# Kernel optimization log

Hardware: AMD Instinct MI355X
Metric: run time of the kernel (lower is better)

## Reference

```python
import jax, jax.numpy as jnp
import numpy as np
from jax import lax

B, D, H, W = 8, 256, 56, 56
DH = 32            # d_head
HEADS = D // DH    # 8
WIN = 7            # window size
TOPK = 8           # top-k windows
DM = 4 * D         # mlp hidden = 1024
EPS = 1e-5


def bn(x, g, b, m, v):
    # inference-mode BatchNorm2d over channel dim of NCHW
    return g[:, None, None] * (x - m[:, None, None]) * lax.rsqrt(v[:, None, None] + EPS) + b[:, None, None]


def conv1x1(x, w):
    return jnp.einsum('bchw,oc->bohw', x, w)


def setup_inputs() -> dict:
    key = jax.random.key(0)
    ks = jax.random.split(key, 24)
    s = 0.05
    return {
        'x': jax.random.normal(ks[0], (B, D, H, W), jnp.float32),
        'g1': jax.random.uniform(ks[1], (D,)) + 0.5,
        'b1': jax.random.normal(ks[2], (D,)) * s,
        'm1': jax.random.normal(ks[3], (D,)) * s,
        'v1': jax.random.uniform(ks[4], (D,)) + 0.5,
        'W_qkv': jax.random.normal(ks[5], (3 * D, D)) * s,
        'W_merge': jax.random.normal(ks[6], (D, D)) * s,
        'b_merge': jax.random.normal(ks[7], (D,)) * s,
        'W1': jax.random.normal(ks[8], (DM, D)) * s,
        'g2': jax.random.uniform(ks[9], (DM,)) + 0.5,
        'b2': jax.random.normal(ks[10], (DM,)) * s,
        'm2': jax.random.normal(ks[11], (DM,)) * s,
        'v2': jax.random.uniform(ks[12], (DM,)) + 0.5,
        'Wdw': jax.random.normal(ks[13], (DM, 1, 3, 3)) * s,
        'g3': jax.random.uniform(ks[14], (DM,)) + 0.5,
        'b3': jax.random.normal(ks[15], (DM,)) * s,
        'm3': jax.random.normal(ks[16], (DM,)) * s,
        'v3': jax.random.uniform(ks[17], (DM,)) + 0.5,
        'W2': jax.random.normal(ks[18], (D, DM)) * s,
        'g4': jax.random.uniform(ks[19], (D,)) + 0.5,
        'b4': jax.random.normal(ks[20], (D,)) * s,
        'm4': jax.random.normal(ks[21], (D,)) * s,
        'v4': jax.random.uniform(ks[22], (D,)) + 0.5,
    }


def _forward(x, g1, b1, m1, v1, W_qkv, W_merge, b_merge,
             W1, g2, b2, m2, v2, Wdw, g3, b3, m3, v3, W2, g4, b4, m4, v4):
    b_, d, Hh, Ww = x.shape
    nh, nw = Hh // WIN, Ww // WIN
    nWnd, ww = nh * nw, WIN * WIN

    # qkv projection: BN -> GELU -> 1x1 conv
    h = jax.nn.gelu(bn(x, g1, b1, m1, v1), approximate=False)
    qkv = conv1x1(h, W_qkv)
    q, k, v = jnp.split(qkv, 3, axis=1)  # each [b, d, H, W]

    def part(t):  # -> [b, heads, nWnd, ww, dh]
        t = t.reshape(b_, HEADS, DH, nh, WIN, nw, WIN)
        return jnp.transpose(t, (0, 1, 3, 5, 4, 6, 2)).reshape(b_, HEADS, nWnd, ww, DH)

    qw, kw, vw = part(q), part(k), part(v)

    # window-level routing: mean-pooled q/k per window, top-k window selection
    def pool(t):  # [b, d, H, W] -> [b, nWnd, d]
        t = t.reshape(b_, d, nh, WIN, nw, WIN).mean(axis=(3, 5))
        return t.reshape(b_, d, nWnd).transpose(0, 2, 1)

    qr, kr = pool(q), pool(k)
    aff = jnp.einsum('bnd,bmd->bnm', qr, kr)        # [b, nWnd, nWnd]
    idx = lax.top_k(aff, TOPK)[1]                    # [b, nWnd, TOPK]

    def gath(t, i):  # t [heads, nWnd, ww, dh], i [nWnd, TOPK]
        return t[:, i]  # [heads, nWnd, TOPK, ww, dh]

    kg = jax.vmap(gath)(kw, idx).reshape(b_, HEADS, nWnd, TOPK * ww, DH)
    vg = jax.vmap(gath)(vw, idx).reshape(b_, HEADS, nWnd, TOPK * ww, DH)

    scores = jnp.einsum('bhnqd,bhnkd->bhnqk', qw, kg) / jnp.sqrt(jnp.float32(DH))
    attn = jax.nn.softmax(scores, axis=-1)
    out = jnp.einsum('bhnqk,bhnkd->bhnqd', attn, vg)  # [b, heads, nWnd, ww, dh]

    # un-partition back to [b, d, H, W]
    out = out.reshape(b_, HEADS, nh, nw, WIN, WIN, DH)
    msg = jnp.transpose(out, (0, 1, 6, 2, 4, 3, 5)).reshape(b_, d, Hh, Ww)

    # merge (1x1 conv with bias) + residual
    x = x + conv1x1(msg, W_merge) + b_merge[None, :, None, None]

    # MB mlp block: 1x1 -> BN -> GELU -> dw3x3 -> BN -> GELU -> 1x1 -> BN
    h2 = conv1x1(x, W1)
    h2 = jax.nn.gelu(bn(h2, g2, b2, m2, v2), approximate=False)
    h2 = lax.conv_general_dilated(h2, Wdw, (1, 1), 'SAME',
                                  feature_group_count=DM,
                                  dimension_numbers=('NCHW', 'OIHW', 'NCHW'))
    h2 = jax.nn.gelu(bn(h2, g3, b3, m3, v3), approximate=False)
    h2 = conv1x1(h2, W2)
    h2 = bn(h2, g4, b4, m4, v4)
    return x + h2


def reference(x, g1, b1, m1, v1, W_qkv, W_merge, b_merge,
              W1, g2, b2, m2, v2, Wdw, g3, b3, m3, v3, W2, g4, b4, m4, v4):
    return _forward(x, g1, b1, m1, v1, W_qkv, W_merge, b_merge,
                    W1, g2, b2, m2, v2, Wdw, g3, b3, m3, v3, W2, g4, b4, m4, v4)
```

## Files before the change

kernel.cpp:

```cpp
#include <hip/hip_runtime.h>
#include <hip/hip_bf16.h>
#include <cstdint>
#include <cstddef>

#define BB 8
#define PP 3136
#define EPSV 1e-5f
#define SCQK 0.17677669529663687f

using bf16x8 = __attribute__((ext_vector_type(8))) short;
using f32x4  = __attribute__((ext_vector_type(4))) float;

__device__ __forceinline__ float bf2f(unsigned short u) {
    union { float f; unsigned int i; } c; c.i = ((unsigned int)u) << 16; return c.f;
}
__device__ __forceinline__ unsigned short f2bf(float f) {
    __hip_bfloat16 h = __float2bfloat16(f);
    union { __hip_bfloat16 h; unsigned short u; } c; c.h = h; return c.u;
}
__device__ __forceinline__ float gelu_f(float t) {
    return 0.5f * t * (1.0f + erff(t * 0.70710678118654752440f));
}
__device__ __forceinline__ float gelu_fast(float x) {
    float z = 1.5957691216057308f * (x + 0.044715f * x * x * x);
    return x / (1.0f + __expf(-z));
}
__device__ __forceinline__ void async16(const void* g, void* s) {
    __builtin_amdgcn_global_load_lds(
        (const __attribute__((address_space(1))) unsigned int*)g,
        (__attribute__((address_space(3))) unsigned int*)s, 16, 0, 0);
}
__device__ __forceinline__ uint4 pack8(const float* v) {
    uint4 o;
    o.x = (unsigned)f2bf(v[0]) | ((unsigned)f2bf(v[1]) << 16);
    o.y = (unsigned)f2bf(v[2]) | ((unsigned)f2bf(v[3]) << 16);
    o.z = (unsigned)f2bf(v[4]) | ((unsigned)f2bf(v[5]) << 16);
    o.w = (unsigned)f2bf(v[6]) | ((unsigned)f2bf(v[7]) << 16);
    return o;
}

__global__ __launch_bounds__(256) void cvt_all_k(
    const float* __restrict__ Wq, const float* __restrict__ Wm,
    const float* __restrict__ W1, const float* __restrict__ W2,
    unsigned short* __restrict__ dq, unsigned short* __restrict__ dm,
    unsigned short* __restrict__ d1, unsigned short* __restrict__ d2)
{
    int i = blockIdx.x * 256 + threadIdx.x;
    if (i < 196608) dq[i] = f2bf(Wq[i]);
    else if (i < 262144) dm[i - 196608] = f2bf(Wm[i - 196608]);
    else if (i < 524288) d1[i - 262144] = f2bf(W1[i - 262144]);
    else d2[i - 524288] = f2bf(W2[i - 524288]);
}

__global__ __launch_bounds__(256) void transin_k(const float* __restrict__ x,
    const float* __restrict__ g1, const float* __restrict__ b1,
    const float* __restrict__ m1, const float* __restrict__ v1,
    float* __restrict__ x_pm, unsigned short* __restrict__ h_bf)
{
    __shared__ float tile[64][65];
    __shared__ float gam[64], bet[64], mu[64], rst[64];
    const int p0 = blockIdx.x * 64, c0 = blockIdx.y * 64, b = blockIdx.z;
    const int t = threadIdx.x;
    if (t < 64) { int c = c0 + t; gam[t] = g1[c]; bet[t] = b1[c]; mu[t] = m1[c]; rst[t] = rsqrtf(v1[c] + EPSV); }
    {
        int cl = t >> 2, px = (t & 3) * 16;
        const float* src = x + ((size_t)(b * 256 + c0 + cl)) * PP + p0 + px;
        #pragma unroll
        for (int i4 = 0; i4 < 4; i4++) {
            float4 r0 = *(const float4*)(src + i4 * 4);
            tile[cl][px + i4*4 + 0] = r0.x; tile[cl][px + i4*4 + 1] = r0.y;
            tile[cl][px + i4*4 + 2] = r0.z; tile[cl][px + i4*4 + 3] = r0.w;
        }
    }
    __syncthreads();
    {
        int pl = t >> 2, cb = (t & 3) * 16;
        float raw[16], hg[16];
        #pragma unroll
        for (int i = 0; i < 16; i++) {
            float vv = tile[cb + i][pl];
            raw[i] = vv;
            hg[i] = gelu_fast(gam[cb + i] * (vv - mu[cb + i]) * rst[cb + i] + bet[cb + i]);
        }
        size_t off = ((size_t)b * PP + p0 + pl) * 256 + c0 + cb;
        float* xd = x_pm + off;
        #pragma unroll
        for (int i4 = 0; i4 < 4; i4++) {
            float4 o; o.x = raw[i4*4]; o.y = raw[i4*4+1]; o.z = raw[i4*4+2]; o.w = raw[i4*4+3];
            *(float4*)(xd + i4 * 4) = o;
        }
        uint4* hd = (uint4*)(h_bf + off);
        hd[0] = pack8(&hg[0]);
        hd[1] = pack8(&hg[8]);
    }
}

template<int EPI>
__global__ __launch_bounds__(256) void gemm_mfma_k(
    const unsigned short* __restrict__ Aact,
    const unsigned short* __restrict__ Wbf,
    const int K, const int Mout,
    void* __restrict__ C1, void* __restrict__ C2,
    const float* __restrict__ e0, const float* __restrict__ e1,
    const float* __restrict__ e2, const float* __restrict__ e3,
    const float* __restrict__ resid)
{
    __shared__ __align__(16) char smem[32768];
    unsigned short* As0 = (unsigned short*)smem;
    unsigned short* Bs0 = (unsigned short*)(smem + 16384);
    float* T = (float*)smem;

    const int tid = threadIdx.x;
    const int w = tid >> 6, lane = tid & 63, g = lane >> 4, l15 = lane & 15;
    const int wm = w >> 1, wn = w & 1;
    const size_t row0 = (size_t)blockIdx.x * 128;
    const int n0 = blockIdx.y * 128;
    const int srow = tid >> 2, scb = tid & 3;

    const f32x4 vzero = {0.f, 0.f, 0.f, 0.f};
    f32x4 acc[4][4];
    #pragma unroll
    for (int mf = 0; mf < 4; mf++)
        #pragma unroll
        for (int nf = 0; nf < 4; nf++) acc[mf][nf] = vzero;

    const int NT = K >> 5;

    auto STAGE = [&](int s) {
        const int k0 = s << 5;
        unsigned short* Ad = As0 + (s & 1) * 4096;
        unsigned short* Bd = Bs0 + (s & 1) * 4096;
        #pragma unroll
        for (int r = 0; r < 2; r++) {
            int row = r * 64 + srow;
            int cbp = scb ^ ((row >> 1) & 3);
            async16(Aact + (row0 + row) * K + k0 + cbp * 8, Ad + r * 2048 + w * 512);
            async16(Wbf + (size_t)(n0 + row) * K + k0 + cbp * 8, Bd + r * 2048 + w * 512);
        }
    };
    auto COMPUTE = [&](int t) {
        const unsigned short* Ab = As0 + (t & 1) * 4096;
        const unsigned short* Bb = Bs0 + (t & 1) * 4096;
        bf16x8 af[4], bfr[4];
        #pragma unroll
        for (int mf = 0; mf < 4; mf++) {
            int row = wm * 64 + mf * 16 + l15;
            int gb = g ^ ((row >> 1) & 3);
            af[mf] = *(const bf16x8*)&Ab[row * 32 + gb * 8];
        }
        #pragma unroll
        for (int nf = 0; nf < 4; nf++) {
            int row = wn * 64 + nf * 16 + l15;
            int gb = g ^ ((row >> 1) & 3);
            bfr[nf] = *(const bf16x8*)&Bb[row * 32 + gb * 8];
        }
        #pragma unroll
        for (int mf = 0; mf < 4; mf++)
            #pragma unroll
            for (int nf = 0; nf < 4; nf++)
                acc[mf][nf] = __builtin_amdgcn_mfma_f32_16x16x32_bf16(af[mf], bfr[nf], acc[mf][nf], 0, 0, 0);
    };

    STAGE(0);
    for (int t = 0; t < NT; ++t) {
        __syncthreads();
        if (t + 1 < NT) STAGE(t + 1);
        COMPUTE(t);
    }

    __syncthreads();
    const int r32 = tid >> 3;
    const int col0 = (tid & 7) * 16;
    #pragma unroll
    for (int p = 0; p < 4; ++p) {
        if (p) __syncthreads();
        if (wm == (p >> 1)) {
            const int mfb = (p & 1) * 2;
            #pragma unroll
            for (int mo = 0; mo < 2; mo++)
                #pragma unroll
                for (int nf = 0; nf < 4; nf++)
                    #pragma unroll
                    for (int r = 0; r < 4; r++)
                        T[(mo * 16 + g * 4 + r) * 132 + wn * 64 + nf * 16 + l15] = acc[mfb + mo][nf][r];
        }
        __syncthreads();
        float vals[16];
        #pragma unroll
        for (int i = 0; i < 4; i++) {
            float4 v = *(const float4*)&T[r32 * 132 + col0 + i * 4];
            vals[i*4+0] = v.x; vals[i*4+1] = v.y; vals[i*4+2] = v.z; vals[i*4+3] = v.w;
        }
        const size_t prow = row0 + p * 32 + r32;
        const int mc0 = n0 + col0;
        const size_t off = prow * Mout + mc0;
        if (EPI == 0) {
            const float s = (mc0 < 256) ? SCQK : 1.0f;
            #pragma unroll
            for (int j = 0; j < 16; j++) vals[j] *= s;
            uint4* dst = (uint4*)((unsigned short*)C1 + off);
            dst[0] = pack8(&vals[0]); dst[1] = pack8(&vals[8]);
        } else if (EPI == 1) {
            #pragma unroll
            for (int i = 0; i < 4; i++) {
                float4 bi = *(const float4*)(e0 + mc0 + i * 4);
                float4 rr = *(const float4*)(resid + off + i * 4);
                vals[i*4+0] += bi.x + rr.x; vals[i*4+1] += bi.y + rr.y;
                vals[i*4+2] += bi.z + rr.z; vals[i*4+3] += bi.w + rr.w;
            }
            float4* d1 = (float4*)((float*)C1 + off);
            #pragma unroll
            for (int i = 0; i < 4; i++) {
                float4 o; o.x = vals[i*4]; o.y = vals[i*4+1]; o.z = vals[i*4+2]; o.w = vals[i*4+3];
                d1[i] = o;
            }
            uint4* d2 = (uint4*)((unsigned short*)C2 + off);
            d2[0] = pack8(&vals[0]); d2[1] = pack8(&vals[8]);
        } else if (EPI == 2) {
            #pragma unroll
            for (int i = 0; i < 4; i++) {
                float4 ga = *(const float4*)(e0 + mc0 + i * 4);
                float4 be = *(const float4*)(e1 + mc0 + i * 4);
                float4 mm = *(const float4*)(e2 + mc0 + i * 4);
                float4 vv = *(const float4*)(e3 + mc0 + i * 4);
                vals[i*4+0] = gelu_fast(ga.x * (vals[i*4+0] - mm.x) * rsqrtf(vv.x + EPSV) + be.x);
                vals[i*4+1] = gelu_fast(ga.y * (vals[i*4+1] - mm.y) * rsqrtf(vv.y + EPSV) + be.y);
                vals[i*4+2] = gelu_fast(ga.z * (vals[i*4+2] - mm.z) * rsqrtf(vv.z + EPSV) + be.z);
                vals[i*4+3] = gelu_fast(ga.w * (vals[i*4+3] - mm.w) * rsqrtf(vv.w + EPSV) + be.w);
            }
            uint4* dst = (uint4*)((unsigned short*)C1 + off);
            dst[0] = pack8(&vals[0]); dst[1] = pack8(&vals[8]);
        } else {
            #pragma unroll
            for (int i = 0; i < 4; i++) {
                float4 ga = *(const float4*)(e0 + mc0 + i * 4);
                float4 be = *(const float4*)(e1 + mc0 + i * 4);
                float4 mm = *(const float4*)(e2 + mc0 + i * 4);
                float4 vv = *(const float4*)(e3 + mc0 + i * 4);
                float4 rr = *(const float4*)(resid + off + i * 4);
                vals[i*4+0] = ga.x * (vals[i*4+0] - mm.x) * rsqrtf(vv.x + EPSV) + be.x + rr.x;
                vals[i*4+1] = ga.y * (vals[i*4+1] - mm.y) * rsqrtf(vv.y + EPSV) + be.y + rr.y;
                vals[i*4+2] = ga.z * (vals[i*4+2] - mm.z) * rsqrtf(vv.z + EPSV) + be.z + rr.z;
                vals[i*4+3] = ga.w * (vals[i*4+3] - mm.w) * rsqrtf(vv.w + EPSV) + be.w + rr.w;
            }
            float4* d1 = (float4*)((float*)C1 + off);
            #pragma unroll
            for (int i = 0; i < 4; i++) {
                float4 o; o.x = vals[i*4]; o.y = vals[i*4+1]; o.z = vals[i*4+2]; o.w = vals[i*4+3];
                d1[i] = o;
            }
        }
    }
}

__global__ __launch_bounds__(256) void poolh_k(const float* __restrict__ x_pm,
    const float* __restrict__ g1, const float* __restrict__ b1,
    const float* __restrict__ m1, const float* __restrict__ v1,
    float* __restrict__ ph)
{
    __shared__ float part[4][256];
    __shared__ float gam[256], bet[256], mu[256], rst[256];
    const int n = blockIdx.x, b = blockIdx.y, t = threadIdx.x;
    gam[t] = g1[t]; bet[t] = b1[t]; mu[t] = m1[t]; rst[t] = rsqrtf(v1[t] + EPSV);
    __syncthreads();
    const int c4 = (t & 63) * 4, pg = t >> 6;
    float s0 = 0.f, s1 = 0.f, s2 = 0.f, s3 = 0.f;
    for (int j = pg; j < 49; j += 4) {
        int p = ((n >> 3) * 7 + j / 7) * 56 + (n & 7) * 7 + j % 7;
        float4 vx = *(const float4*)(x_pm + ((size_t)b * PP + p) * 256 + c4);
        s0 += gelu_f(gam[c4+0] * (vx.x - mu[c4+0]) * rst[c4+0] + bet[c4+0]);
        s1 += gelu_f(gam[c4+1] * (vx.y - mu[c4+1]) * rst[c4+1] + bet[c4+1]);
        s2 += gelu_f(gam[c4+2] * (vx.z - mu[c4+2]) * rst[c4+2] + bet[c4+2]);
        s3 += gelu_f(gam[c4+3] * (vx.w - mu[c4+3]) * rst[c4+3] + bet[c4+3]);
    }
    part[pg][c4 + 0] = s0; part[pg][c4 + 1] = s1; part[pg][c4 + 2] = s2; part[pg][c4 + 3] = s3;
    __syncthreads();
    float tot = part[0][t] + part[1][t] + part[2][t] + part[3][t];
    ph[((size_t)b * 64 + n) * 256 + t] = tot * (1.0f / 49.0f);
}

__global__ __launch_bounds__(256) void qrkr_k(const float* __restrict__ ph,
    const float* __restrict__ Wqkv, float* __restrict__ qr, float* __restrict__ kr)
{
    __shared__ float row[256];
    const int n = blockIdx.x, b = blockIdx.y, t = threadIdx.x;
    row[t] = ph[((size_t)b * 64 + n) * 256 + t];
    __syncthreads();
    const float* wq = Wqkv + (size_t)t * 256;
    const float* wk = Wqkv + (size_t)(256 + t) * 256;
    float aq = 0.f, ak = 0.f;
    #pragma unroll 4
    for (int k = 0; k < 256; k += 4) {
        float4 a4 = *(const float4*)(wq + k);
        float4 b4 = *(const float4*)(wk + k);
        aq += row[k]*a4.x + row[k+1]*a4.y + row[k+2]*a4.z + row[k+3]*a4.w;
        ak += row[k]*b4.x + row[k+1]*b4.y + row[k+2]*b4.z + row[k+3]*b4.w;
    }
    qr[((size_t)b * 64 + n) * 256 + t] = aq;
    kr[((size_t)b * 64 + n) * 256 + t] = ak;
}

__global__ __launch_bounds__(64) void topk_k(const float* __restrict__ qr,
    const float* __restrict__ kr, int* __restrict__ idxb)
{
    const int n = blockIdx.x, b_ = blockIdx.y;
    const int tid = threadIdx.x;
    __shared__ float qrow[256];
    *reinterpret_cast<float4*>(&qrow[tid * 4]) =
        *reinterpret_cast<const float4*>(qr + ((size_t)(b_ * 64) + n) * 256 + tid * 4);
    __syncthreads();
    const float* kp = kr + ((size_t)(b_ * 64) + tid) * 256;
    float av = 0.f;
    #pragma unroll 4
    for (int c = 0; c < 256; c++) av = fmaf(qrow[c], kp[c], av);
    for (int t = 0; t < 8; t++) {
        float v = av; int id = tid;
        #pragma unroll
        for (int off = 32; off; off >>= 1) {
            float v2 = __shfl_xor(v, off);
            int id2 = __shfl_xor(id, off);
            if (v2 > v || (v2 == v && id2 < id)) { v = v2; id = id2; }
        }
        if (tid == 0) idxb[((b_ * 64) + n) * 8 + t] = id;
        if (tid == id) av = -1e30f;
    }
}

__global__ __launch_bounds__(256) void attn_mfma_k(const unsigned short* __restrict__ qkv,
    const int* __restrict__ idxb, unsigned short* __restrict__ msg)
{
    __shared__ __align__(16) unsigned short Vt[32 * 72];
    __shared__ __align__(16) unsigned short Pr[4][16 * 72];
    const int n = blockIdx.x, h = blockIdx.y, b = blockIdx.z;
    const int tid = threadIdx.x;
    const int w = tid >> 6, lane = tid & 63, g = lane >> 4, l15 = lane & 15;

    for (int e = tid; e < 32 * 72; e += 256) Vt[e] = 0;

    const int iq = w * 16 + l15;
    bf16x8 qf = {0, 0, 0, 0, 0, 0, 0, 0};
    if (iq < 49) {
        int p = ((n >> 3) * 7 + iq / 7) * 56 + (n & 7) * 7 + iq % 7;
        qf = *(const bf16x8*)(qkv + ((size_t)b * PP + p) * 768 + h * 32 + g * 8);
    }
    int widx[8];
    {
        const int* ip = idxb + ((b * 64) + n) * 8;
        #pragma unroll
        for (int t = 0; t < 8; t++) widx[t] = ip[t];
    }
    const f32x4 vzero = {0.f, 0.f, 0.f, 0.f};
    f32x4 o0 = vzero, o1 = vzero;
    float mrow = -1e30f, lrow = 0.f;

    const bool act = tid < 196;
    const int jrow = tid >> 2, c8 = (tid & 3) * 8;
    uint4 vv_r = {0,0,0,0};
    auto LOADV = [&](int t) {
        int wsrc = widx[t];
        int p = ((wsrc >> 3) * 7 + jrow / 7) * 56 + (wsrc & 7) * 7 + jrow % 7;
        vv_r = *(const uint4*)(qkv + ((size_t)b * PP + p) * 768 + 512 + h * 32 + c8);
    };
    if (act) LOADV(0);

    for (int t = 0; t < 8; t++) {
        const int wsrc = widx[t];
        const int sy0 = (wsrc >> 3) * 7, sx0 = (wsrc & 7) * 7;
        bf16x8 kf[4];
        #pragma unroll
        for (int nf = 0; nf < 4; nf++) {
            int j = nf * 16 + l15;
            int jc = (j < 49) ? j : 0;
            int p = (sy0 + jc / 7) * 56 + sx0 + jc % 7;
            kf[nf] = *(const bf16x8*)(qkv + ((size_t)b * PP + p) * 768 + 256 + h * 32 + g * 8);
        }
        __syncthreads();
        if (act) {
            const unsigned short* pv = (const unsigned short*)&vv_r;
            #pragma unroll
            for (int jj = 0; jj < 8; jj++) {
                int dh = c8 + jj;
                Vt[dh * 72 + (jrow ^ (((dh >> 3) & 3) << 3))] = pv[jj];
            }
            if (t < 7) LOADV(t + 1);
        }
        __syncthreads();
        f32x4 s[4];
        #pragma unroll
        for (int nf = 0; nf < 4; nf++)
            s[nf] = __builtin_amdgcn_mfma_f32_16x16x32_bf16(kf[nf], qf, vzero, 0, 0, 0);
        float sv[16];
        #pragma unroll
        for (int nf = 0; nf < 4; nf++)
            #pragma unroll
            for (int r = 0; r < 4; r++) {
                int j = nf * 16 + g * 4 + r;
                sv[nf * 4 + r] = (j < 49) ? s[nf][r] : -1e30f;
            }
        float wmx = sv[0];
        #pragma unroll
        for (int e = 1; e < 16; e++) wmx = fmaxf(wmx, sv[e]);
        wmx = fmaxf(wmx, __shfl_xor(wmx, 16));
        wmx = fmaxf(wmx, __shfl_xor(wmx, 32));
        float mn = fmaxf(mrow, wmx);
        float corr = __expf(mrow - mn);
        mrow = mn;
        float rsum = 0.f;
        #pragma unroll
        for (int e = 0; e < 16; e++) { float pe = __expf(sv[e] - mn); sv[e] = pe; rsum += pe; }
        rsum += __shfl_xor(rsum, 16);
        rsum += __shfl_xor(rsum, 32);
        lrow = lrow * corr + rsum;
        #pragma unroll
        for (int r = 0; r < 4; r++) { o0[r] *= corr; o1[r] *= corr; }
        #pragma unroll
        for (int nf = 0; nf < 4; nf++) {
            uint2 pw;
            pw.x = (unsigned)f2bf(sv[nf*4+0]) | ((unsigned)f2bf(sv[nf*4+1]) << 16);
            pw.y = (unsigned)f2bf(sv[nf*4+2]) | ((unsigned)f2bf(sv[nf*4+3]) << 16);
            *(uint2*)&Pr[w][l15 * 72 + nf * 16 + g * 4] = pw;
        }
        asm volatile("s_waitcnt lgkmcnt(0)" ::: "memory");
        __builtin_amdgcn_sched_barrier(0);
        #pragma unroll
        for (int ks = 0; ks < 2; ks++) {
            const int j0 = ks * 32 + g * 8;
            bf16x8 pf  = *(const bf16x8*)&Pr[w][l15 * 72 + j0];
            bf16x8 vf0 = *(const bf16x8*)&Vt[l15 * 72 + (j0 ^ (((l15 >> 3) & 1) << 3))];
            bf16x8 vf1 = *(const bf16x8*)&Vt[(16 + l15) * 72 + (j0 ^ ((2 + (l15 >> 3)) << 3))];
            o0 = __builtin_amdgcn_mfma_f32_16x16x32_bf16(vf0, pf, o0, 0, 0, 0);
            o1 = __builtin_amdgcn_mfma_f32_16x16x32_bf16(vf1, pf, o1, 0, 0, 0);
        }
    }
    if (iq < 49) {
        float inv = 1.0f / lrow;
        int p = ((n >> 3) * 7 + iq / 7) * 56 + (n & 7) * 7 + iq % 7;
        size_t off = ((size_t)b * PP + p) * 256 + h * 32;
        uint2 w0, w1;
        w0.x = (unsigned)f2bf(o0[0]*inv) | ((unsigned)f2bf(o0[1]*inv) << 16);
        w0.y = (unsigned)f2bf(o0[2]*inv) | ((unsigned)f2bf(o0[3]*inv) << 16);
        w1.x = (unsigned)f2bf(o1[0]*inv) | ((unsigned)f2bf(o1[1]*inv) << 16);
        w1.y = (unsigned)f2bf(o1[2]*inv) | ((unsigned)f2bf(o1[3]*inv) << 16);
        *(uint2*)(msg + off + g * 4) = w0;
        *(uint2*)(msg + off + 16 + g * 4) = w1;
    }
}

__global__ __launch_bounds__(256) void dwconv_k(const unsigned short* __restrict__ in,
    const float* __restrict__ w9,
    const float* __restrict__ g3, const float* __restrict__ b3,
    const float* __restrict__ m3, const float* __restrict__ v3,
    unsigned short* __restrict__ out)
{
    __shared__ __align__(16) unsigned short tl[100 * 64];
    const int sx = blockIdx.x % 7, sy = blockIdx.x / 7;
    const int c0 = blockIdx.y * 64, b = blockIdx.z;
    const int t = threadIdx.x;
    for (int e = t; e < 800; e += 256) {
        int pos = e >> 3, c8 = (e & 7) * 8;
        int iy = sy * 8 + pos / 10 - 1, ix = sx * 8 + pos % 10 - 1;
        uint4 val = {0u, 0u, 0u, 0u};
        if (iy >= 0 && iy < 56 && ix >= 0 && ix < 56)
            val = *(const uint4*)(in + ((size_t)b * PP + iy * 56 + ix) * 1024 + c0 + c8);
        *(uint4*)&tl[pos * 64 + c8] = val;
    }
    __syncthreads();
    const int c2 = (t & 31) * 2, pg = t >> 5;
    const int c = c0 + c2;
    float w0[9], w1[9];
    #pragma unroll
    for (int i = 0; i < 9; i++) { w0[i] = w9[c * 9 + i]; w1[i] = w9[(c + 1) * 9 + i]; }
    const float ga0 = g3[c], be0 = b3[c], mu0 = m3[c], rs0 = rsqrtf(v3[c] + EPSV);
    const float ga1 = g3[c+1], be1 = b3[c+1], mu1 = m3[c+1], rs1 = rsqrtf(v3[c+1] + EPSV);
    #pragma unroll
    for (int q = 0; q < 8; q++) {
        int pos = pg * 8 + q, y = pos >> 3, xq = pos & 7;
        float s0 = 0.f, s1 = 0.f;
        #pragma unroll
        for (int dy = 0; dy < 3; dy++)
            #pragma unroll
            for (int dx = 0; dx < 3; dx++) {
                unsigned int u = *(const unsigned int*)&tl[((y + dy) * 10 + xq + dx) * 64 + c2];
                s0 = fmaf(bf2f((unsigned short)(u & 0xffffu)), w0[dy * 3 + dx], s0);
                s1 = fmaf(bf2f((unsigned short)(u >> 16)), w1[dy * 3 + dx], s1);
            }
        float y0 = gelu_fast(ga0 * (s0 - mu0) * rs0 + be0);
        float y1 = gelu_fast(ga1 * (s1 - mu1) * rs1 + be1);
        unsigned int ow = (unsigned int)f2bf(y0) | ((unsigned int)f2bf(y1) << 16);
        size_t off = ((size_t)b * PP + (sy * 8 + y) * 56 + sx * 8 + xq) * 1024 + c;
        *(unsigned int*)&out[off] = ow;
    }
}

__global__ __launch_bounds__(256) void transout_k(const float* __restrict__ out_pm,
    float* __restrict__ dout)
{
    __shared__ float tile[64][65];
    const int p0 = blockIdx.x * 64, c0 = blockIdx.y * 64, b = blockIdx.z;
    const int t = threadIdx.x;
    {
        int pl = t >> 2, cx = (t & 3) * 16;
        const float* src = out_pm + ((size_t)b * PP + p0 + pl) * 256 + c0 + cx;
        #pragma unroll
        for (int i4 = 0; i4 < 4; i4++) {
            float4 vv = *(const float4*)(src + i4 * 4);
            tile[pl][cx + i4*4 + 0] = vv.x; tile[pl][cx + i4*4 + 1] = vv.y;
            tile[pl][cx + i4*4 + 2] = vv.z; tile[pl][cx + i4*4 + 3] = vv.w;
        }
    }
    __syncthreads();
    {
        int cl = t >> 2, px = (t & 3) * 16;
        float* dst = dout + ((size_t)(b * 256 + c0 + cl)) * PP + p0 + px;
        #pragma unroll
        for (int i4 = 0; i4 < 4; i4++) {
            float4 o;
            o.x = tile[px + i4*4 + 0][cl]; o.y = tile[px + i4*4 + 1][cl];
            o.z = tile[px + i4*4 + 2][cl]; o.w = tile[px + i4*4 + 3][cl];
            *(float4*)(dst + i4 * 4) = o;
        }
    }
}

extern "C" void kernel_launch(void* const* d_in, const int* in_sizes, int n_in,
                              void* d_out, int out_size, void* d_ws, size_t ws_size,
                              hipStream_t stream)
{
    const float* x      = (const float*)d_in[0];
    const float* g1     = (const float*)d_in[1];
    const float* b1     = (const float*)d_in[2];
    const float* m1     = (const float*)d_in[3];
    const float* v1     = (const float*)d_in[4];
    const float* Wqkv   = (const float*)d_in[5];
    const float* Wmerge = (const float*)d_in[6];
    const float* bmerge = (const float*)d_in[7];
    const float* W1     = (const float*)d_in[8];
    const float* g2     = (const float*)d_in[9];
    const float* b2     = (const float*)d_in[10];
    const float* m2     = (const float*)d_in[11];
    const float* v2     = (const float*)d_in[12];
    const float* Wdw    = (const float*)d_in[13];
    const float* g3     = (const float*)d_in[14];
    const float* b3     = (const float*)d_in[15];
    const float* m3     = (const float*)d_in[16];
    const float* v3     = (const float*)d_in[17];
    const float* W2     = (const float*)d_in[18];
    const float* g4     = (const float*)d_in[19];
    const float* b4     = (const float*)d_in[20];
    const float* m4     = (const float*)d_in[21];
    const float* v4     = (const float*)d_in[22];

    char* ws = (char*)d_ws;
    float*          x_pm   = (float*)(ws + 0);
    float*          x2_pm  = (float*)(ws + 25690112);
    unsigned short* x2_bf  = (unsigned short*)(ws + 51380224);
    unsigned short* qkv_pm = (unsigned short*)(ws + 64225280);
    unsigned short* msg_pm = (unsigned short*)(ws + 102760448);
    unsigned short* t1     = (unsigned short*)(ws + 115605504);
    unsigned short* h_bf   = t1;
    unsigned short* t2     = (unsigned short*)(ws + 166985728);
    float*          ph     = (float*)(ws + 218365952);
    float*          qr     = (float*)(ws + 218890240);
    float*          kr     = (float*)(ws + 219414528);
    int*            idxb   = (int*)(ws + 219938816);
    unsigned short* Wqkv_b = (unsigned short*)(ws + 219955200);
    unsigned short* Wmrg_b = (unsigned short*)(ws + 220348416);
    unsigned short* W1_b   = (unsigned short*)(ws + 220479488);
    unsigned short* W2_b   = (unsigned short*)(ws + 221003776);
    float*          out_pm = x_pm;
    if (ws_size < 221528064) return;

    cvt_all_k<<<3072, 256, 0, stream>>>(Wqkv, Wmerge, W1, W2, Wqkv_b, Wmrg_b, W1_b, W2_b);
    transin_k<<<dim3(49, 4, BB), 256, 0, stream>>>(x, g1, b1, m1, v1, x_pm, h_bf);
    gemm_mfma_k<0><<<dim3(196, 6), 256, 0, stream>>>(h_bf, Wqkv_b, 256, 768,
        qkv_pm, nullptr, nullptr, nullptr, nullptr, nullptr, nullptr);
    poolh_k<<<dim3(64, BB), 256, 0, stream>>>(x_pm, g1, b1, m1, v1, ph);
    qrkr_k<<<dim3(64, BB), 256, 0, stream>>>(ph, Wqkv, qr, kr);
    topk_k<<<dim3(64, BB), 64, 0, stream>>>(qr, kr, idxb);
    attn_mfma_k<<<dim3(64, 8, BB), 256, 0, stream>>>(qkv_pm, idxb, msg_pm);
    gemm_mfma_k<1><<<dim3(196, 2), 256, 0, stream>>>(msg_pm, Wmrg_b, 256, 256,
        x2_pm, x2_bf, bmerge, nullptr, nullptr, nullptr, x_pm);
    gemm_mfma_k<2><<<dim3(196, 8), 256, 0, stream>>>(x2_bf, W1_b, 256, 1024,
        t1, nullptr, g2, b2, m2, v2, nullptr);
    dwconv_k<<<dim3(49, 16, BB), 256, 0, stream>>>(t1, Wdw, g3, b3, m3, v3, t2);
    gemm_mfma_k<3><<<dim3(196, 2), 256, 0, stream>>>(t2, W2_b, 1024, 256,
        out_pm, nullptr, g4, b4, m4, v4, x2_pm);
    transout_k<<<dim3(49, 4, BB), 256, 0, stream>>>(out_pm, (float*)d_out);
}
```

Baseline: 336.5 us.

## Use 8-wave GEMM blocks and stage attention K tiles through LDS

The MFMA GEMM now launches 512 threads per 128x128 tile, arranged as a 2x4 wave grid. Each wave holds a 64x32 accumulator, which halves per-thread registers and spreads staging loads and epilogue stores over more threads. The attention kernel now loads K rows cooperatively with coalesced uint4 reads into a shared-memory buffer, prefetched alongside V. This replaces per-lane gathered global loads issued inside the loop. The cost is more waves competing for the same LDS and barriers, and extra shared memory in attention.

```diff
diff --git a/kernel.cpp b/kernel.cpp
--- a/kernel.cpp
+++ b/kernel.cpp
@@ -96,7 +96,7 @@
 }
 
 template<int EPI>
-__global__ __launch_bounds__(256) void gemm_mfma_k(
+__global__ __launch_bounds__(512) void gemm_mfma_k(
     const unsigned short* __restrict__ Aact,
     const unsigned short* __restrict__ Wbf,
     const int K, const int Mout,
@@ -112,36 +112,31 @@
 
     const int tid = threadIdx.x;
     const int w = tid >> 6, lane = tid & 63, g = lane >> 4, l15 = lane & 15;
-    const int wm = w >> 1, wn = w & 1;
+    const int wm = w >> 2, wn = w & 3;
     const size_t row0 = (size_t)blockIdx.x * 128;
     const int n0 = blockIdx.y * 128;
     const int srow = tid >> 2, scb = tid & 3;
 
     const f32x4 vzero = {0.f, 0.f, 0.f, 0.f};
-    f32x4 acc[4][4];
+    f32x4 acc[4][2];
     #pragma unroll
     for (int mf = 0; mf < 4; mf++)
         #pragma unroll
-        for (int nf = 0; nf < 4; nf++) acc[mf][nf] = vzero;
+        for (int nf = 0; nf < 2; nf++) acc[mf][nf] = vzero;
 
     const int NT = K >> 5;
+    const int cbp = scb ^ ((srow >> 1) & 3);
+    const int dstoff = (tid & ~63) * 8;
 
     auto STAGE = [&](int s) {
         const int k0 = s << 5;
-        unsigned short* Ad = As0 + (s & 1) * 4096;
-        unsigned short* Bd = Bs0 + (s & 1) * 4096;
-        #pragma unroll
-        for (int r = 0; r < 2; r++) {
-            int row = r * 64 + srow;
-            int cbp = scb ^ ((row >> 1) & 3);
-            async16(Aact + (row0 + row) * K + k0 + cbp * 8, Ad + r * 2048 + w * 512);
-            async16(Wbf + (size_t)(n0 + row) * K + k0 + cbp * 8, Bd + r * 2048 + w * 512);
-        }
+        async16(Aact + (row0 + srow) * K + k0 + cbp * 8, As0 + (s & 1) * 4096 + dstoff);
+        async16(Wbf + (size_t)(n0 + srow) * K + k0 + cbp * 8, Bs0 + (s & 1) * 4096 + dstoff);
     };
     auto COMPUTE = [&](int t) {
         const unsigned short* Ab = As0 + (t & 1) * 4096;
         const unsigned short* Bb = Bs0 + (t & 1) * 4096;
-        bf16x8 af[4], bfr[4];
+        bf16x8 af[4], bfr[2];
         #pragma unroll
         for (int mf = 0; mf < 4; mf++) {
             int row = wm * 64 + mf * 16 + l15;
@@ -149,15 +144,15 @@
             af[mf] = *(const bf16x8*)&Ab[row * 32 + gb * 8];
         }
         #pragma unroll
-        for (int nf = 0; nf < 4; nf++) {
-            int row = wn * 64 + nf * 16 + l15;
+        for (int nf = 0; nf < 2; nf++) {
+            int row = wn * 32 + nf * 16 + l15;
             int gb = g ^ ((row >> 1) & 3);
             bfr[nf] = *(const bf16x8*)&Bb[row * 32 + gb * 8];
         }
         #pragma unroll
         for (int mf = 0; mf < 4; mf++)
             #pragma unroll
-            for (int nf = 0; nf < 4; nf++)
+            for (int nf = 0; nf < 2; nf++)
                 acc[mf][nf] = __builtin_amdgcn_mfma_f32_16x16x32_bf16(af[mf], bfr[nf], acc[mf][nf], 0, 0, 0);
     };
 
@@ -169,8 +164,8 @@
     }
 
     __syncthreads();
-    const int r32 = tid >> 3;
-    const int col0 = (tid & 7) * 16;
+    const int erow = tid >> 4;
+    const int col0 = (tid & 15) * 8;
     #pragma unroll
     for (int p = 0; p < 4; ++p) {
         if (p) __syncthreads();
@@ -179,30 +174,29 @@
             #pragma unroll
             for (int mo = 0; mo < 2; mo++)
                 #pragma unroll
-                for (int nf = 0; nf < 4; nf++)
+                for (int nf = 0; nf < 2; nf++)
                     #pragma unroll
                     for (int r = 0; r < 4; r++)
-                        T[(mo * 16 + g * 4 + r) * 132 + wn * 64 + nf * 16 + l15] = acc[mfb + mo][nf][r];
+                        T[(mo * 16 + g * 4 + r) * 132 + wn * 32 + nf * 16 + l15] = acc[mfb + mo][nf][r];
         }
         __syncthreads();
-        float vals[16];
-        #pragma unroll
-        for (int i = 0; i < 4; i++) {
-            float4 v = *(const float4*)&T[r32 * 132 + col0 + i * 4];
+        float vals[8];
+        #pragma unroll
+        for (int i = 0; i < 2; i++) {
+            float4 v = *(const float4*)&T[erow * 132 + col0 + i * 4];
             vals[i*4+0] = v.x; vals[i*4+1] = v.y; vals[i*4+2] = v.z; vals[i*4+3] = v.w;
         }
-        const size_t prow = row0 + p * 32 + r32;
+        const size_t prow = row0 + p * 32 + erow;
         const int mc0 = n0 + col0;
         const size_t off = prow * Mout + mc0;
         if (EPI == 0) {
             const float s = (mc0 < 256) ? SCQK : 1.0f;
             #pragma unroll
-            for (int j = 0; j < 16; j++) vals[j] *= s;
-            uint4* dst = (uint4*)((unsigned short*)C1 + off);
-            dst[0] = pack8(&vals[0]); dst[1] = pack8(&vals[8]);
+            for (int j = 0; j < 8; j++) vals[j] *= s;
+            *(uint4*)((unsigned short*)C1 + off) = pack8(vals);
         } else if (EPI == 1) {
             #pragma unroll
-            for (int i = 0; i < 4; i++) {
+            for (int i = 0; i < 2; i++) {
                 float4 bi = *(const float4*)(e0 + mc0 + i * 4);
                 float4 rr = *(const float4*)(resid + off + i * 4);
                 vals[i*4+0] += bi.x + rr.x; vals[i*4+1] += bi.y + rr.y;
@@ -210,15 +204,14 @@
             }
             float4* d1 = (float4*)((float*)C1 + off);
             #pragma unroll
-            for (int i = 0; i < 4; i++) {
+            for (int i = 0; i < 2; i++) {
                 float4 o; o.x = vals[i*4]; o.y = vals[i*4+1]; o.z = vals[i*4+2]; o.w = vals[i*4+3];
                 d1[i] = o;
             }
-            uint4* d2 = (uint4*)((unsigned short*)C2 + off);
-            d2[0] = pack8(&vals[0]); d2[1] = pack8(&vals[8]);
+            *(uint4*)((unsigned short*)C2 + off) = pack8(vals);
         } else if (EPI == 2) {
             #pragma unroll
-            for (int i = 0; i < 4; i++) {
+            for (int i = 0; i < 2; i++) {
                 float4 ga = *(const float4*)(e0 + mc0 + i * 4);
                 float4 be = *(const float4*)(e1 + mc0 + i * 4);
                 float4 mm = *(const float4*)(e2 + mc0 + i * 4);
@@ -228,11 +221,10 @@
                 vals[i*4+2] = gelu_fast(ga.z * (vals[i*4+2] - mm.z) * rsqrtf(vv.z + EPSV) + be.z);
                 vals[i*4+3] = gelu_fast(ga.w * (vals[i*4+3] - mm.w) * rsqrtf(vv.w + EPSV) + be.w);
             }
-            uint4* dst = (uint4*)((unsigned short*)C1 + off);
-            dst[0] = pack8(&vals[0]); dst[1] = pack8(&vals[8]);
+            *(uint4*)((unsigned short*)C1 + off) = pack8(vals);
         } else {
             #pragma unroll
-            for (int i = 0; i < 4; i++) {
+            for (int i = 0; i < 2; i++) {
                 float4 ga = *(const float4*)(e0 + mc0 + i * 4);
                 float4 be = *(const float4*)(e1 + mc0 + i * 4);
                 float4 mm = *(const float4*)(e2 + mc0 + i * 4);
@@ -245,7 +237,7 @@
             }
             float4* d1 = (float4*)((float*)C1 + off);
             #pragma unroll
-            for (int i = 0; i < 4; i++) {
+            for (int i = 0; i < 2; i++) {
                 float4 o; o.x = vals[i*4]; o.y = vals[i*4+1]; o.z = vals[i*4+2]; o.w = vals[i*4+3];
                 d1[i] = o;
             }
@@ -329,12 +321,14 @@
 __global__ __launch_bounds__(256) void attn_mfma_k(const unsigned short* __restrict__ qkv,
     const int* __restrict__ idxb, unsigned short* __restrict__ msg)
 {
+    __shared__ __align__(16) unsigned short Ks[64 * 40];
     __shared__ __align__(16) unsigned short Vt[32 * 72];
     __shared__ __align__(16) unsigned short Pr[4][16 * 72];
     const int n = blockIdx.x, h = blockIdx.y, b = blockIdx.z;
     const int tid = threadIdx.x;
     const int w = tid >> 6, lane = tid & 63, g = lane >> 4, l15 = lane & 15;
 
+    for (int e = tid; e < 64 * 40; e += 256) Ks[e] = 0;
     for (int e = tid; e < 32 * 72; e += 256) Vt[e] = 0;
 
     const int iq = w * 16 + l15;
@@ -355,40 +349,35 @@
 
     const bool act = tid < 196;
     const int jrow = tid >> 2, c8 = (tid & 3) * 8;
-    uint4 vv_r = {0,0,0,0};
-    auto LOADV = [&](int t) {
+    uint4 kk_r = {0,0,0,0}, vv_r = {0,0,0,0};
+    auto LOADW = [&](int t) {
         int wsrc = widx[t];
         int p = ((wsrc >> 3) * 7 + jrow / 7) * 56 + (wsrc & 7) * 7 + jrow % 7;
-        vv_r = *(const uint4*)(qkv + ((size_t)b * PP + p) * 768 + 512 + h * 32 + c8);
+        const unsigned short* srcp = qkv + ((size_t)b * PP + p) * 768 + 256 + h * 32 + c8;
+        kk_r = *(const uint4*)srcp;
+        vv_r = *(const uint4*)(srcp + 256);
     };
-    if (act) LOADV(0);
+    if (act) LOADW(0);
 
     for (int t = 0; t < 8; t++) {
-        const int wsrc = widx[t];
-        const int sy0 = (wsrc >> 3) * 7, sx0 = (wsrc & 7) * 7;
-        bf16x8 kf[4];
-        #pragma unroll
-        for (int nf = 0; nf < 4; nf++) {
-            int j = nf * 16 + l15;
-            int jc = (j < 49) ? j : 0;
-            int p = (sy0 + jc / 7) * 56 + sx0 + jc % 7;
-            kf[nf] = *(const bf16x8*)(qkv + ((size_t)b * PP + p) * 768 + 256 + h * 32 + g * 8);
-        }
         __syncthreads();
         if (act) {
+            *(uint4*)&Ks[jrow * 40 + c8] = kk_r;
             const unsigned short* pv = (const unsigned short*)&vv_r;
             #pragma unroll
             for (int jj = 0; jj < 8; jj++) {
                 int dh = c8 + jj;
                 Vt[dh * 72 + (jrow ^ (((dh >> 3) & 3) << 3))] = pv[jj];
             }
-            if (t < 7) LOADV(t + 1);
+            if (t < 7) LOADW(t + 1);
         }
         __syncthreads();
         f32x4 s[4];
         #pragma unroll
-        for (int nf = 0; nf < 4; nf++)
-            s[nf] = __builtin_amdgcn_mfma_f32_16x16x32_bf16(kf[nf], qf, vzero, 0, 0, 0);
+        for (int nf = 0; nf < 4; nf++) {
+            bf16x8 kf = *(const bf16x8*)&Ks[(nf * 16 + l15) * 40 + g * 8];
+            s[nf] = __builtin_amdgcn_mfma_f32_16x16x32_bf16(kf, qf, vzero, 0, 0, 0);
+        }
         float sv[16];
         #pragma unroll
         for (int nf = 0; nf < 4; nf++)
@@ -572,18 +561,18 @@
 
     cvt_all_k<<<3072, 256, 0, stream>>>(Wqkv, Wmerge, W1, W2, Wqkv_b, Wmrg_b, W1_b, W2_b);
     transin_k<<<dim3(49, 4, BB), 256, 0, stream>>>(x, g1, b1, m1, v1, x_pm, h_bf);
-    gemm_mfma_k<0><<<dim3(196, 6), 256, 0, stream>>>(h_bf, Wqkv_b, 256, 768,
+    gemm_mfma_k<0><<<dim3(196, 6), 512, 0, stream>>>(h_bf, Wqkv_b, 256, 768,
         qkv_pm, nullptr, nullptr, nullptr, nullptr, nullptr, nullptr);
     poolh_k<<<dim3(64, BB), 256, 0, stream>>>(x_pm, g1, b1, m1, v1, ph);
     qrkr_k<<<dim3(64, BB), 256, 0, stream>>>(ph, Wqkv, qr, kr);
     topk_k<<<dim3(64, BB), 64, 0, stream>>>(qr, kr, idxb);
     attn_mfma_k<<<dim3(64, 8, BB), 256, 0, stream>>>(qkv_pm, idxb, msg_pm);
-    gemm_mfma_k<1><<<dim3(196, 2), 256, 0, stream>>>(msg_pm, Wmrg_b, 256, 256,
+    gemm_mfma_k<1><<<dim3(196, 2), 512, 0, stream>>>(msg_pm, Wmrg_b, 256, 256,
         x2_pm, x2_bf, bmerge, nullptr, nullptr, nullptr, x_pm);
-    gemm_mfma_k<2><<<dim3(196, 8), 256, 0, stream>>>(x2_bf, W1_b, 256, 1024,
+    gemm_mfma_k<2><<<dim3(196, 8), 512, 0, stream>>>(x2_bf, W1_b, 256, 1024,
         t1, nullptr, g2, b2, m2, v2, nullptr);
     dwconv_k<<<dim3(49, 16, BB), 256, 0, stream>>>(t1, Wdw, g3, b3, m3, v3, t2);
-    gemm_mfma_k<3><<<dim3(196, 2), 256, 0, stream>>>(t2, W2_b, 1024, 256,
+    gemm_mfma_k<3><<<dim3(196, 2), 512, 0, stream>>>(t2, W2_b, 1024, 256,
         out_pm, nullptr, g4, b4, m4, v4, x2_pm);
     transout_k<<<dim3(49, 4, BB), 256, 0, stream>>>(out_pm, (float*)d_out);
 }
```

Measured after the change: 307.8 us. 1.09x faster.
